# Kernel tuning notes

Hardware: AMD Instinct MI355X
Metric: run time of the kernel (lower is better)

## Reference

```python
import jax, jax.numpy as jnp
import numpy as np

N = 8192
D = 64
NEG_INF = -9e15
LEAKY_SLOPE = 0.01  # torch nn.LeakyReLU default


def setup_inputs() -> dict:
    key = jax.random.key(0)
    k1, k2, k3 = jax.random.split(key, 3)
    h = jax.random.normal(k1, (N, D), dtype=jnp.float32)
    adj = jax.random.randint(k2, (N, N), 0, 2, dtype=jnp.int32)
    # xavier_uniform for a: shape (2D, 1), gain=1 -> bound = sqrt(6/(2D+1))
    bound = float(np.sqrt(6.0 / (2 * D + 1)))
    a = jax.random.uniform(k3, (2 * D, 1), dtype=jnp.float32, minval=-bound, maxval=bound)
    return {"h": h, "adj": adj, "a": a}


def reference(h, adj, a):
    # Math identical to cat([h_i, h_j]) @ a: split a into source/target halves.
    a1 = a[:D, 0]  # (D,)
    a2 = a[D:, 0]  # (D,)
    src = h @ a1   # (N,) contribution of h_i
    dst = h @ a2   # (N,) contribution of h_j
    e = src[:, None] + dst[None, :]            # (N, N)
    e = jnp.where(e > 0, e, LEAKY_SLOPE * e)   # leaky relu
    e = jnp.where(adj > 0, e, NEG_INF)         # mask non-edges
    attention = jax.nn.softmax(e, axis=1)      # row softmax over neighbors
    # dropout is inference-mode (training=False) -> identity
    h_prime = attention @ h                    # (N, D)
    return h_prime
```

## Files before the change

### kernel.cpp

```cpp
#include <hip/hip_runtime.h>
#include <hip/hip_bf16.h>

#define NN 8192
#define DD 64
#define SPLIT 4

typedef __attribute__((ext_vector_type(8))) short short8;
typedef __attribute__((ext_vector_type(4))) float f32x4;

__device__ inline ushort f2bf(float f) {
    union { float f; unsigned u; } v; v.f = f;
    unsigned u = v.u;
    unsigned r = (u + 0x7FFFu + ((u >> 16) & 1u)) >> 16;
    return (ushort)r;
}

__global__ __launch_bounds__(256) void srcdst_kernel(
    const float* __restrict__ h, const float* __restrict__ a,
    float* __restrict__ src, float* __restrict__ dst)
{
    int row  = blockIdx.x * 4 + (threadIdx.x >> 6);
    int lane = threadIdx.x & 63;
    float v = h[(size_t)row * DD + lane];
    float s = v * a[lane];
    float t = v * a[DD + lane];
    #pragma unroll
    for (int m = 32; m; m >>= 1) {
        s += __shfl_xor(s, m);
        t += __shfl_xor(t, m);
    }
    if (lane == 0) { src[row] = s; dst[row] = t; }
}

__global__ __launch_bounds__(256) void pack_kernel(
    const float* __restrict__ h, ushort* __restrict__ HB)
{
    int tid = blockIdx.x * 256 + threadIdx.x;
    int e = tid & 7;
    int l = (tid >> 3) & 63;
    int t = (tid >> 9) & 3;
    int c = tid >> 11;
    int row = c * 32 + ((l >> 4) << 3) + e;
    int col = t * 16 + (l & 15);
    HB[tid] = f2bf(h[(size_t)row * DD + col]);
}

__global__ __launch_bounds__(256) void gat_main(
    const int*   __restrict__ adj,
    const float* __restrict__ src,
    const float* __restrict__ dst,
    const ushort* __restrict__ HB,
    float* __restrict__ po,
    float* __restrict__ pl)
{
    int tid  = threadIdx.x;
    int w    = tid >> 6;
    int lane = tid & 63;
    int r    = lane & 15;
    int g    = lane >> 4;
    int ig   = blockIdx.x / SPLIT;
    int sp   = blockIdx.x % SPLIT;
    int i0   = ig * 16;

    short8 lab, uni;
    {
        ushort lv = f2bf((float)r);
        ushort uv = f2bf(1.0f / 32.0f);
        #pragma unroll
        for (int e = 0; e < 8; ++e) { lab[e] = (short)lv; uni[e] = (short)uv; }
    }
    f32x4 zf = {};
    f32x4 t_row = __builtin_amdgcn_mfma_f32_16x16x32_bf16(lab, uni, zf, 0, 0, 0);
    f32x4 t_col = __builtin_amdgcn_mfma_f32_16x16x32_bf16(uni, lab, zf, 0, 0, 0);
    int rowlab[4], collab[4];
    #pragma unroll
    for (int q = 0; q < 4; ++q) {
        rowlab[q] = (int)(t_row[q] + 0.5f);
        collab[q] = (int)(t_col[q] + 0.5f);
    }

    float srcv = src[i0 + r];
    f32x4 acc[4] = {};
    float lsum = 0.f;

    const int jbase = sp * (NN / SPLIT) + w * (NN / SPLIT / 4);
    const int* adjrow = adj + (size_t)(i0 + r) * NN;

    for (int c = 0; c < (NN / SPLIT / 4) / 32; ++c) {
        int j0 = jbase + c * 32;
        int gc = j0 >> 5;
        const int jg = j0 + g * 8;
        int4   a0 = *reinterpret_cast<const int4*>(adjrow + jg);
        int4   a1 = *reinterpret_cast<const int4*>(adjrow + jg + 4);
        float4 d0 = *reinterpret_cast<const float4*>(dst + jg);
        float4 d1 = *reinterpret_cast<const float4*>(dst + jg + 4);
        int   am[8] = {a0.x, a0.y, a0.z, a0.w, a1.x, a1.y, a1.z, a1.w};
        float dv[8] = {d0.x, d0.y, d0.z, d0.w, d1.x, d1.y, d1.z, d1.w};
        short8 af;
        #pragma unroll
        for (int e = 0; e < 8; ++e) {
            float ev = srcv + dv[e];
            ev = fmaxf(ev, 0.01f * ev);
            float pe = (am[e] > 0) ? __expf(ev) : 0.f;
            lsum += pe;
            af[e] = (short)f2bf(pe);
        }
        const ushort* hb = HB + (size_t)gc * 2048 + lane * 8;
        #pragma unroll
        for (int t = 0; t < 4; ++t) {
            short8 bf = *reinterpret_cast<const short8*>(hb + t * 512);
            acc[t] = __builtin_amdgcn_mfma_f32_16x16x32_bf16(af, bf, acc[t], 0, 0, 0);
        }
    }

    lsum += __shfl_xor(lsum, 16);
    lsum += __shfl_xor(lsum, 32);

    __shared__ float o_sh[4][16][64];
    __shared__ float l_sh[4][16];
    #pragma unroll
    for (int t = 0; t < 4; ++t)
        #pragma unroll
        for (int q = 0; q < 4; ++q)
            o_sh[w][rowlab[q]][t * 16 + collab[q]] = acc[t][q];
    if (g == 0) l_sh[w][r] = lsum;
    __syncthreads();

    float* pob = po + ((size_t)blockIdx.x) * 16 * 64;
    for (int it = tid; it < 16 * 64; it += 256) {
        int row = it >> 6, d = it & 63;
        pob[it] = o_sh[0][row][d] + o_sh[1][row][d] + o_sh[2][row][d] + o_sh[3][row][d];
    }
    if (tid < 16)
        pl[(size_t)blockIdx.x * 16 + tid] =
            l_sh[0][tid] + l_sh[1][tid] + l_sh[2][tid] + l_sh[3][tid];
}

__global__ __launch_bounds__(256) void reduce_kernel(
    const float* __restrict__ po, const float* __restrict__ pl,
    float* __restrict__ out)
{
    int idx = blockIdx.x * 256 + threadIdx.x;
    int row = idx >> 6;
    int d   = idx & 63;
    int ig  = row >> 4;
    int r   = row & 15;
    float o = 0.f, l = 0.f;
    #pragma unroll
    for (int sp = 0; sp < SPLIT; ++sp) {
        int b = ig * SPLIT + sp;
        o += po[((size_t)b * 16 + r) * 64 + d];
        l += pl[(size_t)b * 16 + r];
    }
    out[idx] = o / l;
}

extern "C" void kernel_launch(void* const* d_in, const int* in_sizes, int n_in,
                              void* d_out, int out_size, void* d_ws, size_t ws_size,
                              hipStream_t stream) {
    const float* h   = (const float*)d_in[0];
    const int*   adj = (const int*)d_in[1];
    const float* a   = (const float*)d_in[2];
    float* out = (float*)d_out;

    char* ws = (char*)d_ws;
    float*  src = (float*)ws;
    float*  dst = src + NN;
    ushort* HB  = (ushort*)(ws + (1u << 16));
    float*  po  = (float*)(ws + (2u << 20));
    float*  pl  = (float*)(ws + (12u << 20));

    srcdst_kernel<<<NN / 4, 256, 0, stream>>>(h, a, src, dst);
    pack_kernel<<<(NN * DD) / 256, 256, 0, stream>>>(h, HB);
    gat_main<<<(NN / 16) * SPLIT, 256, 0, stream>>>(adj, src, dst, HB, po, pl);
    reduce_kernel<<<(NN * DD) / 256, 256, 0, stream>>>(po, pl, out);
}
```

Measured before the change: 81.34 us.

## Compute softmax denominator via extra MFMA ones-column and trim VALU work

Adds a fifth B tile to the packed H layout that holds a ones column, so the row sum of exp weights falls out of an extra MFMA instead of scalar adds and cross-lane shuffles. Also switches the bf16 conversion to the hardware cast, packs the row/column label arrays into bitfields, uses incremented pointers, and sets a launch-bounds occupancy hint. This cuts VALU work in the memory-bound inner loop. In exchange it adds one more MFMA and more HB traffic per chunk, and the denominator now sums bf16-rounded weights, which changes numerics slightly.

```diff
diff --git a/kernel.cpp b/kernel.cpp
--- a/kernel.cpp
+++ b/kernel.cpp
@@ -13,6 +13,11 @@
     unsigned u = v.u;
     unsigned r = (u + 0x7FFFu + ((u >> 16) & 1u)) >> 16;
     return (ushort)r;
+}
+
+__device__ inline short f2bf_hw(float f) {
+    __bf16 b = (__bf16)f;
+    return (short)__builtin_bit_cast(unsigned short, b);
 }
 
 __global__ __launch_bounds__(256) void srcdst_kernel(
@@ -36,16 +41,23 @@
     const float* __restrict__ h, ushort* __restrict__ HB)
 {
     int tid = blockIdx.x * 256 + threadIdx.x;
-    int e = tid & 7;
-    int l = (tid >> 3) & 63;
-    int t = (tid >> 9) & 3;
-    int c = tid >> 11;
-    int row = c * 32 + ((l >> 4) << 3) + e;
-    int col = t * 16 + (l & 15);
-    HB[tid] = f2bf(h[(size_t)row * DD + col]);
+    int c   = tid / 2560;
+    int rem = tid - c * 2560;
+    int t   = rem >> 9;
+    int l   = (rem >> 3) & 63;
+    int e   = rem & 7;
+    ushort v;
+    if (t < 4) {
+        int row = c * 32 + ((l >> 4) << 3) + e;
+        int col = t * 16 + (l & 15);
+        v = f2bf(h[(size_t)row * DD + col]);
+    } else {
+        v = ((l & 15) == 0) ? (ushort)0x3F80 : (ushort)0;
+    }
+    HB[tid] = v;
 }
 
-__global__ __launch_bounds__(256) void gat_main(
+__global__ __launch_bounds__(256, 8) void gat_main(
     const int*   __restrict__ adj,
     const float* __restrict__ src,
     const float* __restrict__ dst,
@@ -72,28 +84,26 @@
     f32x4 zf = {};
     f32x4 t_row = __builtin_amdgcn_mfma_f32_16x16x32_bf16(lab, uni, zf, 0, 0, 0);
     f32x4 t_col = __builtin_amdgcn_mfma_f32_16x16x32_bf16(uni, lab, zf, 0, 0, 0);
-    int rowlab[4], collab[4];
+    int rcode = 0, ccode = 0;
     #pragma unroll
     for (int q = 0; q < 4; ++q) {
-        rowlab[q] = (int)(t_row[q] + 0.5f);
-        collab[q] = (int)(t_col[q] + 0.5f);
+        rcode |= ((int)(t_row[q] + 0.5f)) << (8 * q);
+        ccode |= ((int)(t_col[q] + 0.5f)) << (8 * q);
     }
 
     float srcv = src[i0 + r];
-    f32x4 acc[4] = {};
-    float lsum = 0.f;
+    f32x4 acc[5] = {};
 
     const int jbase = sp * (NN / SPLIT) + w * (NN / SPLIT / 4);
-    const int* adjrow = adj + (size_t)(i0 + r) * NN;
+    const int*    ap = adj + (size_t)(i0 + r) * NN + jbase + g * 8;
+    const float*  dp = dst + jbase + g * 8;
+    const ushort* hp = HB + (size_t)(jbase >> 5) * 2560 + lane * 8;
 
     for (int c = 0; c < (NN / SPLIT / 4) / 32; ++c) {
-        int j0 = jbase + c * 32;
-        int gc = j0 >> 5;
-        const int jg = j0 + g * 8;
-        int4   a0 = *reinterpret_cast<const int4*>(adjrow + jg);
-        int4   a1 = *reinterpret_cast<const int4*>(adjrow + jg + 4);
-        float4 d0 = *reinterpret_cast<const float4*>(dst + jg);
-        float4 d1 = *reinterpret_cast<const float4*>(dst + jg + 4);
+        int4   a0 = *reinterpret_cast<const int4*>(ap);
+        int4   a1 = *reinterpret_cast<const int4*>(ap + 4);
+        float4 d0 = *reinterpret_cast<const float4*>(dp);
+        float4 d1 = *reinterpret_cast<const float4*>(dp + 4);
         int   am[8] = {a0.x, a0.y, a0.z, a0.w, a1.x, a1.y, a1.z, a1.w};
         float dv[8] = {d0.x, d0.y, d0.z, d0.w, d1.x, d1.y, d1.z, d1.w};
         short8 af;
@@ -102,19 +112,15 @@
             float ev = srcv + dv[e];
             ev = fmaxf(ev, 0.01f * ev);
             float pe = (am[e] > 0) ? __expf(ev) : 0.f;
-            lsum += pe;
-            af[e] = (short)f2bf(pe);
+            af[e] = f2bf_hw(pe);
         }
-        const ushort* hb = HB + (size_t)gc * 2048 + lane * 8;
         #pragma unroll
-        for (int t = 0; t < 4; ++t) {
-            short8 bf = *reinterpret_cast<const short8*>(hb + t * 512);
+        for (int t = 0; t < 5; ++t) {
+            short8 bf = *reinterpret_cast<const short8*>(hp + t * 512);
             acc[t] = __builtin_amdgcn_mfma_f32_16x16x32_bf16(af, bf, acc[t], 0, 0, 0);
         }
+        ap += 32; dp += 32; hp += 2560;
     }
-
-    lsum += __shfl_xor(lsum, 16);
-    lsum += __shfl_xor(lsum, 32);
 
     __shared__ float o_sh[4][16][64];
     __shared__ float l_sh[4][16];
@@ -122,8 +128,11 @@
     for (int t = 0; t < 4; ++t)
         #pragma unroll
         for (int q = 0; q < 4; ++q)
-            o_sh[w][rowlab[q]][t * 16 + collab[q]] = acc[t][q];
-    if (g == 0) l_sh[w][r] = lsum;
+            o_sh[w][(rcode >> (8 * q)) & 15][t * 16 + ((ccode >> (8 * q)) & 15)] = acc[t][q];
+    #pragma unroll
+    for (int q = 0; q < 4; ++q)
+        if (((ccode >> (8 * q)) & 15) == 0)
+            l_sh[w][(rcode >> (8 * q)) & 15] = acc[4][q];
     __syncthreads();
 
     float* pob = po + ((size_t)blockIdx.x) * 16 * 64;
@@ -171,7 +180,7 @@
     float*  pl  = (float*)(ws + (12u << 20));
 
     srcdst_kernel<<<NN / 4, 256, 0, stream>>>(h, a, src, dst);
-    pack_kernel<<<(NN * DD) / 256, 256, 0, stream>>>(h, HB);
+    pack_kernel<<<(NN / 32) * 2560 / 256, 256, 0, stream>>>(h, HB);
     gat_main<<<(NN / 16) * SPLIT, 256, 0, stream>>>(adj, src, dst, HB, po, pl);
     reduce_kernel<<<(NN * DD) / 256, 256, 0, stream>>>(po, pl, out);
 }
```

Measured after the change: 85.74 us. 5.4% more time.

## Stage adjacency tiles through LDS with coalesced row loads and double buffering

Applied to the files above, without the earlier changes.

The adjacency mask is now loaded with a coalesced pattern, where each group of four lanes reads 128 contiguous bytes of one row. It is staged into a per-wave double-buffered LDS tile and the next chunk is prefetched while the current one is computed. The main loop is fully unrolled, bf16 conversion uses the hardware cast, labels are packed into ints, and launch bounds request 8 blocks per CU. The LDS buffer is reused for the final reduction, with an added barrier. Costs are extra LDS traffic and register pressure from the prefetch and unrolling. The staging relies on wave-level lockstep, with no barrier between the LDS write and the later read.

```diff
diff --git a/kernel.cpp b/kernel.cpp
--- a/kernel.cpp
+++ b/kernel.cpp
@@ -13,6 +13,11 @@
     unsigned u = v.u;
     unsigned r = (u + 0x7FFFu + ((u >> 16) & 1u)) >> 16;
     return (ushort)r;
+}
+
+__device__ inline short f2bf_hw(float f) {
+    __bf16 b = (__bf16)f;
+    return (short)__builtin_bit_cast(unsigned short, b);
 }
 
 __global__ __launch_bounds__(256) void srcdst_kernel(
@@ -45,7 +50,7 @@
     HB[tid] = f2bf(h[(size_t)row * DD + col]);
 }
 
-__global__ __launch_bounds__(256) void gat_main(
+__global__ __launch_bounds__(256, 8) void gat_main(
     const int*   __restrict__ adj,
     const float* __restrict__ src,
     const float* __restrict__ dst,
@@ -62,6 +67,10 @@
     int sp   = blockIdx.x % SPLIT;
     int i0   = ig * 16;
 
+    __shared__ char smem[18432];
+    __shared__ float l_sh[4][16];
+    int* stw = (int*)smem + w * 1152;
+
     short8 lab, uni;
     {
         ushort lv = f2bf((float)r);
@@ -72,11 +81,11 @@
     f32x4 zf = {};
     f32x4 t_row = __builtin_amdgcn_mfma_f32_16x16x32_bf16(lab, uni, zf, 0, 0, 0);
     f32x4 t_col = __builtin_amdgcn_mfma_f32_16x16x32_bf16(uni, lab, zf, 0, 0, 0);
-    int rowlab[4], collab[4];
+    int rcode = 0, ccode = 0;
     #pragma unroll
     for (int q = 0; q < 4; ++q) {
-        rowlab[q] = (int)(t_row[q] + 0.5f);
-        collab[q] = (int)(t_col[q] + 0.5f);
+        rcode |= ((int)(t_row[q] + 0.5f)) << (8 * q);
+        ccode |= ((int)(t_col[q] + 0.5f)) << (8 * q);
     }
 
     float srcv = src[i0 + r];
@@ -84,17 +93,35 @@
     float lsum = 0.f;
 
     const int jbase = sp * (NN / SPLIT) + w * (NN / SPLIT / 4);
-    const int* adjrow = adj + (size_t)(i0 + r) * NN;
-
-    for (int c = 0; c < (NN / SPLIT / 4) / 32; ++c) {
-        int j0 = jbase + c * 32;
-        int gc = j0 >> 5;
-        const int jg = j0 + g * 8;
-        int4   a0 = *reinterpret_cast<const int4*>(adjrow + jg);
-        int4   a1 = *reinterpret_cast<const int4*>(adjrow + jg + 4);
-        float4 d0 = *reinterpret_cast<const float4*>(dst + jg);
-        float4 d1 = *reinterpret_cast<const float4*>(dst + jg + 4);
-        int   am[8] = {a0.x, a0.y, a0.z, a0.w, a1.x, a1.y, a1.z, a1.w};
+    int srow = lane >> 2;
+    int sg   = lane & 3;
+    const int*    gsrc = adj + (size_t)(i0 + srow) * NN + jbase + sg * 4;
+    const float*  dp   = dst + jbase + g * 8;
+    const ushort* hp   = HB + (size_t)(jbase >> 5) * 2048 + lane * 8;
+
+    {
+        int4 A0 = *reinterpret_cast<const int4*>(gsrc);
+        int4 A1 = *reinterpret_cast<const int4*>(gsrc + 16);
+        gsrc += 32;
+        *reinterpret_cast<int4*>(stw + srow * 36 + sg * 4)      = A0;
+        *reinterpret_cast<int4*>(stw + srow * 36 + sg * 4 + 16) = A1;
+    }
+
+    #pragma unroll
+    for (int c = 0; c < 16; ++c) {
+        int4 nA0, nA1;
+        if (c < 15) {
+            nA0 = *reinterpret_cast<const int4*>(gsrc);
+            nA1 = *reinterpret_cast<const int4*>(gsrc + 16);
+            gsrc += 32;
+        }
+        const int* mb = stw + (c & 1) * 576 + r * 36 + g * 8;
+        int4 m0 = *reinterpret_cast<const int4*>(mb);
+        int4 m1 = *reinterpret_cast<const int4*>(mb + 4);
+        float4 d0 = *reinterpret_cast<const float4*>(dp);
+        float4 d1 = *reinterpret_cast<const float4*>(dp + 4);
+        dp += 32;
+        int   am[8] = {m0.x, m0.y, m0.z, m0.w, m1.x, m1.y, m1.z, m1.w};
         float dv[8] = {d0.x, d0.y, d0.z, d0.w, d1.x, d1.y, d1.z, d1.w};
         short8 af;
         #pragma unroll
@@ -103,26 +130,31 @@
             ev = fmaxf(ev, 0.01f * ev);
             float pe = (am[e] > 0) ? __expf(ev) : 0.f;
             lsum += pe;
-            af[e] = (short)f2bf(pe);
-        }
-        const ushort* hb = HB + (size_t)gc * 2048 + lane * 8;
+            af[e] = f2bf_hw(pe);
+        }
         #pragma unroll
         for (int t = 0; t < 4; ++t) {
-            short8 bf = *reinterpret_cast<const short8*>(hb + t * 512);
+            short8 bf = *reinterpret_cast<const short8*>(hp + t * 512);
             acc[t] = __builtin_amdgcn_mfma_f32_16x16x32_bf16(af, bf, acc[t], 0, 0, 0);
+        }
+        hp += 2048;
+        if (c < 15) {
+            int* wb = stw + ((c + 1) & 1) * 576 + srow * 36 + sg * 4;
+            *reinterpret_cast<int4*>(wb)      = nA0;
+            *reinterpret_cast<int4*>(wb + 16) = nA1;
         }
     }
 
     lsum += __shfl_xor(lsum, 16);
     lsum += __shfl_xor(lsum, 32);
 
-    __shared__ float o_sh[4][16][64];
-    __shared__ float l_sh[4][16];
+    __syncthreads();
+    float (*o_sh)[16][64] = reinterpret_cast<float (*)[16][64]>(smem);
     #pragma unroll
     for (int t = 0; t < 4; ++t)
         #pragma unroll
         for (int q = 0; q < 4; ++q)
-            o_sh[w][rowlab[q]][t * 16 + collab[q]] = acc[t][q];
+            o_sh[w][(rcode >> (8 * q)) & 15][t * 16 + ((ccode >> (8 * q)) & 15)] = acc[t][q];
     if (g == 0) l_sh[w][r] = lsum;
     __syncthreads();
 
```

Result: slower. 82.99 us (+2.0%).
